# Kernel optimization log

Hardware: AMD Instinct MI355X
Metric: run time of the kernel (lower is better)

## Reference

```python
import jax, jax.numpy as jnp
import numpy as np

N_EMBD = 384
HEAD_SIZE = 64
B, T = 16, 2048


def setup_inputs() -> dict:
    key = jax.random.key(0)
    ks = jax.random.split(key, 7)
    s = 1.0 / np.sqrt(N_EMBD)
    return {
        "x": jax.random.normal(ks[0], (B, T, N_EMBD), dtype=jnp.float32),
        "Wq": jax.random.uniform(ks[1], (N_EMBD, HEAD_SIZE), jnp.float32, -s, s),
        "bq": jax.random.uniform(ks[2], (HEAD_SIZE,), jnp.float32, -s, s),
        "Wk": jax.random.uniform(ks[3], (N_EMBD, HEAD_SIZE), jnp.float32, -s, s),
        "bk": jax.random.uniform(ks[4], (HEAD_SIZE,), jnp.float32, -s, s),
        "Wv": jax.random.uniform(ks[5], (N_EMBD, HEAD_SIZE), jnp.float32, -s, s),
        "bv": jax.random.uniform(ks[6], (HEAD_SIZE,), jnp.float32, -s, s),
    }


def reference(x, Wq, bq, Wk, bk, Wv, bv):
    # QKV projections: [B,T,C] @ [C,H] -> [B,T,H]
    q = x @ Wq + bq
    k = x @ Wk + bk
    v = x @ Wv + bv
    scale = k.shape[-1] ** (-0.5)
    # NOTE: original forward applies NO causal mask (tril buffer unused).
    scores = jnp.einsum("bqh,bkh->bqk", q, k) * scale  # [B,T,T]
    wmap = jax.nn.softmax(scores, axis=-1)
    # dropout is identity in eval mode
    out = jnp.einsum("bqk,bkh->bqh", wmap, v)  # [B,T,H]
    return out
```

## Files before the change

### kernel.cpp

```cpp
#include <hip/hip_runtime.h>
#include <hip/hip_bf16.h>
#include <cstdint>

typedef unsigned short u16;
typedef __attribute__((ext_vector_type(8))) short short8;
typedef __attribute__((ext_vector_type(4))) short short4v;
typedef __attribute__((ext_vector_type(4))) float f32x4;

#define MFMA16(a, b, c) __builtin_amdgcn_mfma_f32_16x16x32_bf16((a), (b), (c), 0, 0, 0)

constexpr int Bn   = 16;
constexpr int Tn   = 2048;
constexpr int Cn   = 384;
constexpr int Hn   = 64;
constexpr long NTOK = (long)Bn * Tn;
constexpr long NELT = NTOK * Hn;
constexpr int SPLITS = 3;

#define QSCALE 0.18033688011112042f

__device__ __forceinline__ u16 f2bf(float f) {
  union { float f; uint32_t u; } c; c.f = f;
  uint32_t u = c.u;
  return (u16)((u + 0x7fffu + ((u >> 16) & 1u)) >> 16);
}

__device__ __forceinline__ uint32_t pkbf(float a, float b) {
  uint32_t d;
  asm("v_cvt_pk_bf16_f32 %0, %1, %2" : "=v"(d) : "v"(a), "v"(b));
  return d;
}

__device__ __forceinline__ short8 ldx8(const float* p) {
  const float4 f0 = *reinterpret_cast<const float4*>(p);
  const float4 f1 = *reinterpret_cast<const float4*>(p + 4);
  union { short8 s8; uint32_t u[4]; } r;
  r.u[0] = pkbf(f0.x, f0.y); r.u[1] = pkbf(f0.z, f0.w);
  r.u[2] = pkbf(f1.x, f1.y); r.u[3] = pkbf(f1.z, f1.w);
  return r.s8;
}

__device__ __forceinline__ void gl16(const u16* g, const u16* l) {
  __builtin_amdgcn_global_load_lds(
      (const __attribute__((address_space(1))) void*)g,
      (__attribute__((address_space(3))) void*)l, 16, 0, 0);
}

__global__ __launch_bounds__(256) void wtrans(
    const float* __restrict__ Wq, const float* __restrict__ Wk,
    const float* __restrict__ Wv, u16* __restrict__ wtd)
{
  __shared__ u16 tile[64][65];
  const int m  = blockIdx.x / 6;
  const int kc = blockIdx.x % 6;
  const float* W = (m == 0) ? Wq : (m == 1) ? Wk : Wv;
  const int t = threadIdx.x;

  {
    const int kr = t >> 2, seg = t & 3;
    const float* src = W + (size_t)(kc * 64 + kr) * Hn + seg * 16;
    #pragma unroll
    for (int j = 0; j < 4; ++j) {
      const float4 f = *reinterpret_cast<const float4*>(src + j * 4);
      u16* p = &tile[kr][seg * 16 + j * 4];
      p[0] = f2bf(f.x); p[1] = f2bf(f.y); p[2] = f2bf(f.z); p[3] = f2bf(f.w);
    }
  }
  __syncthreads();
  {
    const int hr = t >> 2, seg = t & 3;
    union { short8 s; u16 u[8]; } o0, o1;
    #pragma unroll
    for (int j = 0; j < 8; ++j) o0.u[j] = tile[seg * 16 + j][hr];
    #pragma unroll
    for (int j = 0; j < 8; ++j) o1.u[j] = tile[seg * 16 + 8 + j][hr];
    u16* dst = wtd + ((size_t)m * 64 + hr) * Cn + kc * 64 + seg * 16;
    *reinterpret_cast<short8*>(dst)     = o0.s;
    *reinterpret_cast<short8*>(dst + 8) = o1.s;
  }
}

__global__ __launch_bounds__(256, 2) void qkv_proj(
    const float* __restrict__ x, const u16* __restrict__ wtd,
    const float* __restrict__ bq, const float* __restrict__ bk,
    const float* __restrict__ bv,
    u16* __restrict__ oq, u16* __restrict__ ok, u16* __restrict__ ovt)
{
  __shared__ u16 wbuf[3][3 * 64 * 64];

  const int t    = threadIdx.x;
  const int lane = t & 63;
  const int w    = t >> 6;
  const int l15  = lane & 15;
  const int lh   = lane >> 4;
  const long r0  = (long)blockIdx.x * 64;

  int srcoff[6];
  #pragma unroll
  for (int i = 0; i < 6; ++i) {
    const int g = i * 256 + t;
    const int r = g >> 3, c = g & 7;
    srcoff[i] = r * Cn + ((c ^ (r & 7)) << 3);
  }
  const int ldsb = w * 64 * 8;

  const float* xrow = x + (r0 + w * 16 + l15) * Cn;

  const int cks0 = ((lh)     ^ (l15 & 7)) << 3;
  const int cks1 = ((lh + 4) ^ (l15 & 7)) << 3;

  f32x4 acc[3][4];
  #pragma unroll
  for (int m = 0; m < 3; ++m)
    #pragma unroll
    for (int n = 0; n < 4; ++n) acc[m][n] = f32x4{0.f, 0.f, 0.f, 0.f};

  #pragma unroll
  for (int i = 0; i < 6; ++i)
    gl16(wtd + srcoff[i], &wbuf[0][(i * 256) * 8 + ldsb]);
  short8 aCur0 = ldx8(xrow + lh * 8);
  short8 aCur1 = ldx8(xrow + 32 + lh * 8);
  #pragma unroll
  for (int i = 0; i < 6; ++i)
    gl16(wtd + 64 + srcoff[i], &wbuf[1][(i * 256) * 8 + ldsb]);
  short8 aNx10 = ldx8(xrow + 64 + lh * 8);
  short8 aNx11 = ldx8(xrow + 96 + lh * 8);
  short8 aNx20, aNx21;
  asm volatile("s_waitcnt vmcnt(14)" ::: "memory");
  __builtin_amdgcn_s_barrier();
  __builtin_amdgcn_sched_barrier(0);

  for (int kc = 0; kc < 6; ++kc) {
    const int cb = kc % 3;
    const int sb = (kc + 2) % 3;
    if (kc + 2 < 6) {
      #pragma unroll
      for (int i = 0; i < 6; ++i)
        gl16(wtd + (kc + 2) * 64 + srcoff[i], &wbuf[sb][(i * 256) * 8 + ldsb]);
      const float* p = xrow + (kc + 2) * 64 + lh * 8;
      aNx20 = ldx8(p);
      aNx21 = ldx8(p + 32);
    }

    const u16* wc = &wbuf[cb][0];
    #pragma unroll
    for (int m = 0; m < 3; ++m)
      #pragma unroll
      for (int n = 0; n < 4; ++n) {
        const int row = m * 64 + n * 16 + l15;
        const short8 b0 = *reinterpret_cast<const short8*>(&wc[row * 64 + cks0]);
        acc[m][n] = MFMA16(aCur0, b0, acc[m][n]);
        const short8 b1 = *reinterpret_cast<const short8*>(&wc[row * 64 + cks1]);
        acc[m][n] = MFMA16(aCur1, b1, acc[m][n]);
      }

    if (kc + 1 < 6) {
      if (kc + 2 < 6) asm volatile("s_waitcnt vmcnt(14)" ::: "memory");
      else            asm volatile("s_waitcnt vmcnt(4)"  ::: "memory");
      __builtin_amdgcn_s_barrier();
      __builtin_amdgcn_sched_barrier(0);
      aCur0 = aNx10; aCur1 = aNx11;
      aNx10 = aNx20; aNx11 = aNx21;
    }
  }

  {
    const float* bias[2] = {bq, bk};
    u16*         dst[2]  = {oq, ok};
    const float  scl[2]  = {QSCALE, 1.0f};
    #pragma unroll
    for (int m = 0; m < 2; ++m) {
      #pragma unroll
      for (int n = 0; n < 4; ++n) {
        int col = n * 16 + l15;
        float bb = bias[m][col];
        #pragma unroll
        for (int r = 0; r < 4; ++r) {
          int row = lh * 4 + r;
          dst[m][(r0 + w * 16 + row) * Hn + col] = f2bf((acc[m][n][r] + bb) * scl[m]);
        }
      }
    }
  }
  {
    const long g    = r0 + w * 16 + lh * 4;
    const long bidx = g >> 11;
    const long tloc = g & 2047;
    const int  u    = (int)(tloc & 63);
    const long tb   = tloc & ~63L;
    const int  slotb = 32 * ((u >> 5) & 1) + 8 * ((u >> 2) & 3) + 4 * ((u >> 4) & 1);
    #pragma unroll
    for (int n = 0; n < 4; ++n) {
      int col = n * 16 + l15;
      float bb = bv[col];
      short4v pk;
      #pragma unroll
      for (int r = 0; r < 4; ++r) pk[r] = (short)f2bf(acc[2][n][r] + bb);
      *reinterpret_cast<short4v*>(ovt + (bidx * Hn + col) * Tn + tb + slotb) = pk;
    }
  }
}

__global__ __launch_bounds__(256, 3) void flash_attn(
    const u16* __restrict__ q, const u16* __restrict__ k,
    const u16* __restrict__ vt, float* __restrict__ opart,
    float* __restrict__ lpart)
{
  __shared__ u16 kbuf[3][64 * 64];
  __shared__ u16 vbuf[3][64 * 64];

  const int t    = threadIdx.x;
  const int lane = t & 63;
  const int w    = t >> 6;
  const int l15  = lane & 15;
  const int lh   = lane >> 4;
  const int swz_id = (blockIdx.x & 7) * 96 + (blockIdx.x >> 3);
  const int b     = swz_id / 48;
  const int rsw   = swz_id % 48;
  const int split = rsw / 16;
  const int qt    = rsw % 16;
  const long rowbase = (long)b * Tn + qt * 128;
  const int it0 = (split * 32) / 3;
  const int it1 = ((split + 1) * 32) / 3;

  short8 aq[2][2];
  #pragma unroll
  for (int qg = 0; qg < 2; ++qg) {
    const u16* qrow = q + (rowbase + w * 32 + qg * 16 + l15) * Hn;
    aq[qg][0] = *reinterpret_cast<const short8*>(qrow + lh * 8);
    aq[qg][1] = *reinterpret_cast<const short8*>(qrow + 32 + lh * 8);
  }

  union { short8 s8; uint32_t u[4]; } ON;
  #pragma unroll
  for (int i = 0; i < 4; ++i) ON.u[i] = 0x3F803F80u;

  f32x4 o[2][4];
  #pragma unroll
  for (int qg = 0; qg < 2; ++qg)
    #pragma unroll
    for (int m = 0; m < 4; ++m) o[qg][m] = f32x4{0.f, 0.f, 0.f, 0.f};
  f32x4 ls0 = f32x4{0.f, 0.f, 0.f, 0.f};
  f32x4 ls1 = f32x4{0.f, 0.f, 0.f, 0.f};

  const u16* kb_g = k  + (long)b * Tn * Hn;
  const u16* vb_g = vt + (long)b * Hn * Tn;

  const int g0 = t, g1 = 256 + t;
  const int r0g = g0 >> 3, c0g = g0 & 7;
  const int r1g = g1 >> 3, c1g = g1 & 7;
  const long ksrc0 = (long)r0g * Hn + ((c0g ^ (r0g & 7)) << 3);
  const long ksrc1 = (long)r1g * Hn + ((c1g ^ (r1g & 7)) << 3);
  const long vsrc0 = (long)r0g * Tn + ((c0g ^ (r0g & 7)) << 3);
  const long vsrc1 = (long)r1g * Tn + ((c1g ^ (r1g & 7)) << 3);
  const int wb0 = w * 64 * 8;
  const int wb1 = wb0 + 256 * 8;

  const int swz  = l15 & 7;
  const int cks0 = ((0 * 4 + lh) ^ swz) << 3;
  const int cks1 = ((1 * 4 + lh) ^ swz) << 3;
  const int rfr  = l15 * 64;

  {
    const u16* kt = kb_g + (long)it0 * 64 * Hn;
    const u16* vp = vb_g + it0 * 64;
    gl16(kt + ksrc0, &kbuf[0][wb0]);
    gl16(kt + ksrc1, &kbuf[0][wb1]);
    gl16(vp + vsrc0, &vbuf[0][wb0]);
    gl16(vp + vsrc1, &vbuf[0][wb1]);
    const u16* kt1 = kb_g + (long)(it0 + 1) * 64 * Hn;
    const u16* vp1 = vb_g + (it0 + 1) * 64;
    gl16(kt1 + ksrc0, &kbuf[1][wb0]);
    gl16(kt1 + ksrc1, &kbuf[1][wb1]);
    gl16(vp1 + vsrc0, &vbuf[1][wb0]);
    gl16(vp1 + vsrc1, &vbuf[1][wb1]);
  }
  asm volatile("s_waitcnt vmcnt(4)" ::: "memory");
  __builtin_amdgcn_s_barrier();
  __builtin_amdgcn_sched_barrier(0);

  for (int it = it0; it < it1; ++it) {
    const int cb = (it - it0) % 3;
    const int sb = (it - it0 + 2) % 3;
    if (it + 2 < it1) {
      const u16* kt = kb_g + (long)(it + 2) * 64 * Hn;
      const u16* vp = vb_g + (it + 2) * 64;
      gl16(kt + ksrc0, &kbuf[sb][wb0]);
      gl16(kt + ksrc1, &kbuf[sb][wb1]);
      gl16(vp + vsrc0, &vbuf[sb][wb0]);
      gl16(vp + vsrc1, &vbuf[sb][wb1]);
    }

    const u16* kc  = &kbuf[cb][0];
    const u16* vcb = &vbuf[cb][0];

    f32x4 s0[4], s1[4];
    #pragma unroll
    for (int n = 0; n < 4; ++n) { s0[n] = f32x4{0.f,0.f,0.f,0.f}; s1[n] = f32x4{0.f,0.f,0.f,0.f}; }
    #pragma unroll
    for (int n = 0; n < 4; ++n) {
      const short8 ak0 = *reinterpret_cast<const short8*>(&kc[n * 1024 + rfr + cks0]);
      const short8 ak1 = *reinterpret_cast<const short8*>(&kc[n * 1024 + rfr + cks1]);
      s0[n] = MFMA16(ak0, aq[0][0], s0[n]);
      s0[n] = MFMA16(ak1, aq[0][1], s0[n]);
      s1[n] = MFMA16(ak0, aq[1][0], s1[n]);
      s1[n] = MFMA16(ak1, aq[1][1], s1[n]);
    }

    #pragma unroll
    for (int n = 0; n < 4; ++n)
      #pragma unroll
      for (int r = 0; r < 4; ++r) {
        s0[n][r] = __builtin_amdgcn_exp2f(s0[n][r]);
        s1[n][r] = __builtin_amdgcn_exp2f(s1[n][r]);
      }

    union { short8 s8; uint32_t u[4]; } B00, B01, B10, B11;
    B00.u[0] = pkbf(s0[0][0], s0[0][1]); B00.u[1] = pkbf(s0[0][2], s0[0][3]);
    B00.u[2] = pkbf(s0[1][0], s0[1][1]); B00.u[3] = pkbf(s0[1][2], s0[1][3]);
    B01.u[0] = pkbf(s0[2][0], s0[2][1]); B01.u[1] = pkbf(s0[2][2], s0[2][3]);
    B01.u[2] = pkbf(s0[3][0], s0[3][1]); B01.u[3] = pkbf(s0[3][2], s0[3][3]);
    B10.u[0] = pkbf(s1[0][0], s1[0][1]); B10.u[1] = pkbf(s1[0][2], s1[0][3]);
    B10.u[2] = pkbf(s1[1][0], s1[1][1]); B10.u[3] = pkbf(s1[1][2], s1[1][3]);
    B11.u[0] = pkbf(s1[2][0], s1[2][1]); B11.u[1] = pkbf(s1[2][2], s1[2][3]);
    B11.u[2] = pkbf(s1[3][0], s1[3][1]); B11.u[3] = pkbf(s1[3][2], s1[3][3]);

    #pragma unroll
    for (int m = 0; m < 4; ++m) {
      const short8 av0 = *reinterpret_cast<const short8*>(&vcb[m * 1024 + rfr + cks0]);
      const short8 av1 = *reinterpret_cast<const short8*>(&vcb[m * 1024 + rfr + cks1]);
      o[0][m] = MFMA16(av0, B00.s8, o[0][m]);
      o[0][m] = MFMA16(av1, B01.s8, o[0][m]);
      o[1][m] = MFMA16(av0, B10.s8, o[1][m]);
      o[1][m] = MFMA16(av1, B11.s8, o[1][m]);
    }
    ls0 = MFMA16(ON.s8, B00.s8, ls0);
    ls0 = MFMA16(ON.s8, B01.s8, ls0);
    ls1 = MFMA16(ON.s8, B10.s8, ls1);
    ls1 = MFMA16(ON.s8, B11.s8, ls1);

    if (it + 1 < it1) {
      if (it + 2 < it1) asm volatile("s_waitcnt vmcnt(4)" ::: "memory");
      else              asm volatile("s_waitcnt vmcnt(0)" ::: "memory");
      __builtin_amdgcn_s_barrier();
      __builtin_amdgcn_sched_barrier(0);
    }
  }

  #pragma unroll
  for (int qg = 0; qg < 2; ++qg) {
    const float tot = (qg == 0) ? ls0[0] : ls1[0];
    const long qrow = rowbase + w * 32 + qg * 16 + l15;
    float* od = opart + ((long)split * NELT) + qrow * Hn;
    #pragma unroll
    for (int m = 0; m < 4; ++m) {
      float4 vv;
      vv.x = o[qg][m][0]; vv.y = o[qg][m][1]; vv.z = o[qg][m][2]; vv.w = o[qg][m][3];
      *reinterpret_cast<float4*>(od + m * 16 + lh * 4) = vv;
    }
    if (lh == 0) lpart[(long)split * NTOK + qrow] = tot;
  }
}

__global__ __launch_bounds__(256) void combine(
    const float* __restrict__ op, const float* __restrict__ lp,
    float* __restrict__ out)
{
  const long idx  = (long)blockIdx.x * 256 + threadIdx.x;
  const long base = idx * 4;
  const long row  = base >> 6;
  float4 acc = *reinterpret_cast<const float4*>(op + base);
  float lsum = lp[row];
  #pragma unroll
  for (int s = 1; s < SPLITS; ++s) {
    const float4 c = *reinterpret_cast<const float4*>(op + s * NELT + base);
    acc.x += c.x; acc.y += c.y; acc.z += c.z; acc.w += c.w;
    lsum += lp[s * NTOK + row];
  }
  const float linv = 1.0f / lsum;
  float4 r;
  r.x = acc.x * linv; r.y = acc.y * linv; r.z = acc.z * linv; r.w = acc.w * linv;
  *reinterpret_cast<float4*>(out + base) = r;
}

extern "C" void kernel_launch(void* const* d_in, const int* in_sizes, int n_in,
                              void* d_out, int out_size, void* d_ws, size_t ws_size,
                              hipStream_t stream) {
  const float* x  = (const float*)d_in[0];
  const float* Wq = (const float*)d_in[1];
  const float* bq = (const float*)d_in[2];
  const float* Wk = (const float*)d_in[3];
  const float* bk = (const float*)d_in[4];
  const float* Wv = (const float*)d_in[5];
  const float* bv = (const float*)d_in[6];
  float* out = (float*)d_out;

  u16* qs  = (u16*)d_ws;
  u16* ks  = qs + NELT;
  u16* vs  = ks + NELT;
  u16* wtd = vs + NELT;
  float* op = (float*)(wtd + 3 * 64 * Cn);
  float* lp = op + (long)SPLITS * NELT;

  hipLaunchKernelGGL(wtrans, dim3(18), dim3(256), 0, stream, Wq, Wk, Wv, wtd);
  hipLaunchKernelGGL(qkv_proj, dim3((int)(NTOK / 64)), dim3(256), 0, stream,
                     x, wtd, bq, bk, bv, qs, ks, vs);
  hipLaunchKernelGGL(flash_attn, dim3(16 * 16 * SPLITS), dim3(256), 0, stream,
                     qs, ks, vs, op, lp);
  hipLaunchKernelGGL(combine, dim3((int)(NELT / 4 / 256)), dim3(256), 0, stream,
                     op, lp, out);
}
```

Measured before the change: 54.26 us.

## Use 8 waves per attention block, one 16-row query group each

The flash attention block grows from 256 to 512 threads. Each of the 8 waves now owns 16 query rows instead of 32, so per-wave register state (Q fragments, O accumulators, score tiles) is halved. Each thread issues one K and one V tile load per stage instead of two, with the vmcnt waits adjusted to match. The aim is higher occupancy and more latency hiding, at the cost of each LDS K/V fragment being reused by fewer MFMAs per wave read.

```diff
diff --git a/kernel.cpp b/kernel.cpp
--- a/kernel.cpp
+++ b/kernel.cpp
@@ -201,7 +201,7 @@
   }
 }
 
-__global__ __launch_bounds__(256, 3) void flash_attn(
+__global__ __launch_bounds__(512, 6) void flash_attn(
     const u16* __restrict__ q, const u16* __restrict__ k,
     const u16* __restrict__ vt, float* __restrict__ opart,
     float* __restrict__ lpart)
@@ -223,38 +223,29 @@
   const int it0 = (split * 32) / 3;
   const int it1 = ((split + 1) * 32) / 3;
 
-  short8 aq[2][2];
-  #pragma unroll
-  for (int qg = 0; qg < 2; ++qg) {
-    const u16* qrow = q + (rowbase + w * 32 + qg * 16 + l15) * Hn;
-    aq[qg][0] = *reinterpret_cast<const short8*>(qrow + lh * 8);
-    aq[qg][1] = *reinterpret_cast<const short8*>(qrow + 32 + lh * 8);
+  short8 aq0, aq1;
+  {
+    const u16* qrow = q + (rowbase + w * 16 + l15) * Hn;
+    aq0 = *reinterpret_cast<const short8*>(qrow + lh * 8);
+    aq1 = *reinterpret_cast<const short8*>(qrow + 32 + lh * 8);
   }
 
   union { short8 s8; uint32_t u[4]; } ON;
   #pragma unroll
   for (int i = 0; i < 4; ++i) ON.u[i] = 0x3F803F80u;
 
-  f32x4 o[2][4];
-  #pragma unroll
-  for (int qg = 0; qg < 2; ++qg)
-    #pragma unroll
-    for (int m = 0; m < 4; ++m) o[qg][m] = f32x4{0.f, 0.f, 0.f, 0.f};
-  f32x4 ls0 = f32x4{0.f, 0.f, 0.f, 0.f};
-  f32x4 ls1 = f32x4{0.f, 0.f, 0.f, 0.f};
+  f32x4 o[4];
+  #pragma unroll
+  for (int m = 0; m < 4; ++m) o[m] = f32x4{0.f, 0.f, 0.f, 0.f};
+  f32x4 ls = f32x4{0.f, 0.f, 0.f, 0.f};
 
   const u16* kb_g = k  + (long)b * Tn * Hn;
   const u16* vb_g = vt + (long)b * Hn * Tn;
 
-  const int g0 = t, g1 = 256 + t;
-  const int r0g = g0 >> 3, c0g = g0 & 7;
-  const int r1g = g1 >> 3, c1g = g1 & 7;
-  const long ksrc0 = (long)r0g * Hn + ((c0g ^ (r0g & 7)) << 3);
-  const long ksrc1 = (long)r1g * Hn + ((c1g ^ (r1g & 7)) << 3);
-  const long vsrc0 = (long)r0g * Tn + ((c0g ^ (r0g & 7)) << 3);
-  const long vsrc1 = (long)r1g * Tn + ((c1g ^ (r1g & 7)) << 3);
-  const int wb0 = w * 64 * 8;
-  const int wb1 = wb0 + 256 * 8;
+  const int rg = t >> 3, cg = t & 7;
+  const long ksrc = (long)rg * Hn + ((cg ^ (rg & 7)) << 3);
+  const long vsrc = (long)rg * Tn + ((cg ^ (rg & 7)) << 3);
+  const int wbase = w * 64 * 8;
 
   const int swz  = l15 & 7;
   const int cks0 = ((0 * 4 + lh) ^ swz) << 3;
@@ -262,20 +253,12 @@
   const int rfr  = l15 * 64;
 
   {
-    const u16* kt = kb_g + (long)it0 * 64 * Hn;
-    const u16* vp = vb_g + it0 * 64;
-    gl16(kt + ksrc0, &kbuf[0][wb0]);
-    gl16(kt + ksrc1, &kbuf[0][wb1]);
-    gl16(vp + vsrc0, &vbuf[0][wb0]);
-    gl16(vp + vsrc1, &vbuf[0][wb1]);
-    const u16* kt1 = kb_g + (long)(it0 + 1) * 64 * Hn;
-    const u16* vp1 = vb_g + (it0 + 1) * 64;
-    gl16(kt1 + ksrc0, &kbuf[1][wb0]);
-    gl16(kt1 + ksrc1, &kbuf[1][wb1]);
-    gl16(vp1 + vsrc0, &vbuf[1][wb0]);
-    gl16(vp1 + vsrc1, &vbuf[1][wb1]);
-  }
-  asm volatile("s_waitcnt vmcnt(4)" ::: "memory");
+    gl16(kb_g + (long)it0 * 64 * Hn + ksrc, &kbuf[0][wbase]);
+    gl16(vb_g + it0 * 64 + vsrc,            &vbuf[0][wbase]);
+    gl16(kb_g + (long)(it0 + 1) * 64 * Hn + ksrc, &kbuf[1][wbase]);
+    gl16(vb_g + (it0 + 1) * 64 + vsrc,            &vbuf[1][wbase]);
+  }
+  asm volatile("s_waitcnt vmcnt(2)" ::: "memory");
   __builtin_amdgcn_s_barrier();
   __builtin_amdgcn_sched_barrier(0);
 
@@ -283,79 +266,62 @@
     const int cb = (it - it0) % 3;
     const int sb = (it - it0 + 2) % 3;
     if (it + 2 < it1) {
-      const u16* kt = kb_g + (long)(it + 2) * 64 * Hn;
-      const u16* vp = vb_g + (it + 2) * 64;
-      gl16(kt + ksrc0, &kbuf[sb][wb0]);
-      gl16(kt + ksrc1, &kbuf[sb][wb1]);
-      gl16(vp + vsrc0, &vbuf[sb][wb0]);
-      gl16(vp + vsrc1, &vbuf[sb][wb1]);
+      gl16(kb_g + (long)(it + 2) * 64 * Hn + ksrc, &kbuf[sb][wbase]);
+      gl16(vb_g + (it + 2) * 64 + vsrc,            &vbuf[sb][wbase]);
     }
 
     const u16* kc  = &kbuf[cb][0];
     const u16* vcb = &vbuf[cb][0];
 
-    f32x4 s0[4], s1[4];
-    #pragma unroll
-    for (int n = 0; n < 4; ++n) { s0[n] = f32x4{0.f,0.f,0.f,0.f}; s1[n] = f32x4{0.f,0.f,0.f,0.f}; }
+    f32x4 s[4];
+    #pragma unroll
+    for (int n = 0; n < 4; ++n) s[n] = f32x4{0.f, 0.f, 0.f, 0.f};
     #pragma unroll
     for (int n = 0; n < 4; ++n) {
       const short8 ak0 = *reinterpret_cast<const short8*>(&kc[n * 1024 + rfr + cks0]);
+      s[n] = MFMA16(ak0, aq0, s[n]);
       const short8 ak1 = *reinterpret_cast<const short8*>(&kc[n * 1024 + rfr + cks1]);
-      s0[n] = MFMA16(ak0, aq[0][0], s0[n]);
-      s0[n] = MFMA16(ak1, aq[0][1], s0[n]);
-      s1[n] = MFMA16(ak0, aq[1][0], s1[n]);
-      s1[n] = MFMA16(ak1, aq[1][1], s1[n]);
+      s[n] = MFMA16(ak1, aq1, s[n]);
     }
 
     #pragma unroll
     for (int n = 0; n < 4; ++n)
       #pragma unroll
-      for (int r = 0; r < 4; ++r) {
-        s0[n][r] = __builtin_amdgcn_exp2f(s0[n][r]);
-        s1[n][r] = __builtin_amdgcn_exp2f(s1[n][r]);
-      }
-
-    union { short8 s8; uint32_t u[4]; } B00, B01, B10, B11;
-    B00.u[0] = pkbf(s0[0][0], s0[0][1]); B00.u[1] = pkbf(s0[0][2], s0[0][3]);
-    B00.u[2] = pkbf(s0[1][0], s0[1][1]); B00.u[3] = pkbf(s0[1][2], s0[1][3]);
-    B01.u[0] = pkbf(s0[2][0], s0[2][1]); B01.u[1] = pkbf(s0[2][2], s0[2][3]);
-    B01.u[2] = pkbf(s0[3][0], s0[3][1]); B01.u[3] = pkbf(s0[3][2], s0[3][3]);
-    B10.u[0] = pkbf(s1[0][0], s1[0][1]); B10.u[1] = pkbf(s1[0][2], s1[0][3]);
-    B10.u[2] = pkbf(s1[1][0], s1[1][1]); B10.u[3] = pkbf(s1[1][2], s1[1][3]);
-    B11.u[0] = pkbf(s1[2][0], s1[2][1]); B11.u[1] = pkbf(s1[2][2], s1[2][3]);
-    B11.u[2] = pkbf(s1[3][0], s1[3][1]); B11.u[3] = pkbf(s1[3][2], s1[3][3]);
+      for (int r = 0; r < 4; ++r)
+        s[n][r] = __builtin_amdgcn_exp2f(s[n][r]);
+
+    union { short8 s8; uint32_t u[4]; } B0, B1;
+    B0.u[0] = pkbf(s[0][0], s[0][1]); B0.u[1] = pkbf(s[0][2], s[0][3]);
+    B0.u[2] = pkbf(s[1][0], s[1][1]); B0.u[3] = pkbf(s[1][2], s[1][3]);
+    B1.u[0] = pkbf(s[2][0], s[2][1]); B1.u[1] = pkbf(s[2][2], s[2][3]);
+    B1.u[2] = pkbf(s[3][0], s[3][1]); B1.u[3] = pkbf(s[3][2], s[3][3]);
 
     #pragma unroll
     for (int m = 0; m < 4; ++m) {
       const short8 av0 = *reinterpret_cast<const short8*>(&vcb[m * 1024 + rfr + cks0]);
+      o[m] = MFMA16(av0, B0.s8, o[m]);
       const short8 av1 = *reinterpret_cast<const short8*>(&vcb[m * 1024 + rfr + cks1]);
-      o[0][m] = MFMA16(av0, B00.s8, o[0][m]);
-      o[0][m] = MFMA16(av1, B01.s8, o[0][m]);
-      o[1][m] = MFMA16(av0, B10.s8, o[1][m]);
-      o[1][m] = MFMA16(av1, B11.s8, o[1][m]);
-    }
-    ls0 = MFMA16(ON.s8, B00.s8, ls0);
-    ls0 = MFMA16(ON.s8, B01.s8, ls0);
-    ls1 = MFMA16(ON.s8, B10.s8, ls1);
-    ls1 = MFMA16(ON.s8, B11.s8, ls1);
+      o[m] = MFMA16(av1, B1.s8, o[m]);
+    }
+    ls = MFMA16(ON.s8, B0.s8, ls);
+    ls = MFMA16(ON.s8, B1.s8, ls);
 
     if (it + 1 < it1) {
-      if (it + 2 < it1) asm volatile("s_waitcnt vmcnt(4)" ::: "memory");
+      if (it + 2 < it1) asm volatile("s_waitcnt vmcnt(2)" ::: "memory");
       else              asm volatile("s_waitcnt vmcnt(0)" ::: "memory");
       __builtin_amdgcn_s_barrier();
       __builtin_amdgcn_sched_barrier(0);
     }
   }
 
-  #pragma unroll
-  for (int qg = 0; qg < 2; ++qg) {
-    const float tot = (qg == 0) ? ls0[0] : ls1[0];
-    const long qrow = rowbase + w * 32 + qg * 16 + l15;
+  {
+    const float tot = ls[0];
+    const long qrow = rowbase + w * 16 + l15;
     float* od = opart + ((long)split * NELT) + qrow * Hn;
     #pragma unroll
     for (int m = 0; m < 4; ++m) {
       float4 vv;
-      vv.x = o[qg][m][0]; vv.y = o[qg][m][1]; vv.z = o[qg][m][2]; vv.w = o[qg][m][3];
+      vv.x = o[m][0]; vv.y = o[m][1]; vv.z = o[m][2]; vv.w = o[m][3];
       *reinterpret_cast<float4*>(od + m * 16 + lh * 4) = vv;
     }
     if (lh == 0) lpart[(long)split * NTOK + qrow] = tot;
@@ -405,7 +371,7 @@
   hipLaunchKernelGGL(wtrans, dim3(18), dim3(256), 0, stream, Wq, Wk, Wv, wtd);
   hipLaunchKernelGGL(qkv_proj, dim3((int)(NTOK / 64)), dim3(256), 0, stream,
                      x, wtd, bq, bk, bv, qs, ks, vs);
-  hipLaunchKernelGGL(flash_attn, dim3(16 * 16 * SPLITS), dim3(256), 0, stream,
+  hipLaunchKernelGGL(flash_attn, dim3(16 * 16 * SPLITS), dim3(512), 0, stream,
                      qs, ks, vs, op, lp);
   hipLaunchKernelGGL(combine, dim3((int)(NELT / 4 / 256)), dim3(256), 0, stream,
                      op, lp, out);
```

New measurement: 55.15 us. Within noise of the previous version (+1.7%).
